# Performance work log

Hardware: AMD Instinct MI355X
Metric: run time of the kernel (lower is better)

The kernel has to match this reference:

```python
import jax, jax.numpy as jnp
import numpy as np

HIDDEN = 1024
NUM_HEADS = 16
INDEXER_HEADS = 4
D_IDX = 32
K_BASE = 512
K_MIN = 32
K_MAX = 1024
ROPE_BASE = 10000
SINK = 4


def setup_inputs() -> dict:
    key = jax.random.key(0)
    ks = jax.random.split(key, 12)
    std = 0.02
    B, T, C = 1, 2048, HIDDEN
    inp = {
        "x": jax.random.normal(ks[0], (B, T, C), jnp.float32),
        "W_Iq": jax.random.normal(ks[1], (INDEXER_HEADS * D_IDX, C), jnp.float32) * std,
        "W_Ik": jax.random.normal(ks[2], (INDEXER_HEADS * D_IDX, C), jnp.float32) * std,
        "W_Iw": jax.random.normal(ks[3], (INDEXER_HEADS, C), jnp.float32) * std,
        "gate_bias": jnp.zeros((INDEXER_HEADS,), jnp.float32),
        "head_importance_bias": jnp.zeros((NUM_HEADS,), jnp.float32),
        "W_q": jax.random.normal(ks[4], (C, C), jnp.float32) * std,
        "W_k": jax.random.normal(ks[5], (C, C), jnp.float32) * std,
        "W_v": jax.random.normal(ks[6], (C, C), jnp.float32) * std,
        "W_gv": jax.random.normal(ks[7], (C, C), jnp.float32) * std,
        "W_go": jax.random.normal(ks[8], (C, C), jnp.float32) * std,
        "W_o": jax.random.normal(ks[9], (C, C), jnp.float32) * std,
    }
    return inp


def _apply_rotary(x, cos_e, sin_e):
    # x: [B,T,H,hd]; cos_e/sin_e: [1,T,1,hd/2] (the [..., ::2] slice of cat(freqs,freqs))
    x1, x2 = x[..., ::2], x[..., 1::2]
    return jnp.concatenate((x1 * cos_e - x2 * sin_e, x1 * sin_e + x2 * cos_e), axis=-1)


def _gsa_forward(x, W_Iq, W_Ik, W_Iw, gate_bias, head_importance_bias,
                 W_q, W_k, W_v, W_gv, W_go, W_o):
    B, T, C = x.shape
    H = NUM_HEADS
    HI = INDEXER_HEADS
    hd = C // H
    hpi = H // HI

    # ----- lightning indexer -----
    q_I = (x @ W_Iq.T).reshape(B, T, HI, D_IDX)
    k_I = (x @ W_Ik.T).reshape(B, T, HI, D_IDX)
    w = jax.nn.sigmoid(x @ W_Iw.T)                       # [B,T,HI]

    match_logits = jnp.einsum('bqhd,bkhd->bhqk', q_I, k_I)  # [B,HI,T,T]
    match_logits = match_logits + gate_bias[None, :, None, None]
    match_gate = jax.nn.sigmoid(match_logits)
    w_exp = jnp.transpose(w, (0, 2, 1))[..., None]       # [B,HI,T,1]
    imp_per_indexer = w_exp * match_gate                 # [B,HI,T,T]

    importance = jnp.repeat(imp_per_indexer, hpi, axis=1)  # [B,H,T,T]
    importance = importance * jax.nn.sigmoid(head_importance_bias)[None, :, None, None]

    pos = jnp.arange(T)
    causal = pos[:, None] >= pos[None, :]                # [T,T]
    imp_masked = jnp.where(causal[None, None], importance, 0.0)

    # adaptive k_t (eval path: variance_ema == 1.0)
    var_t = jnp.var(imp_masked, axis=-1)                 # [B,H,T], biased
    k_t = jnp.clip(jnp.floor(K_BASE * var_t / 1.0), K_MIN, K_MAX).astype(jnp.int32)

    imp_sel = jnp.where(causal[None, None], importance, -jnp.inf)
    if T > SINK:
        imp_sel = imp_sel.at[..., :SINK].set(jnp.inf)    # attention sinks always selected

    # static k_limit upper bound (>= torch's dynamic min(T, max(k_t.max(), sink)));
    # entries past k_t are masked out by keep_in_topk, so result is identical
    k_limit = min(T, K_MAX)
    _, top_idx = jax.lax.top_k(imp_sel, k_limit)         # [B,H,T,k_limit]
    keep = jnp.arange(k_limit)[None, None, None, :] < k_t[..., None]

    b_ix = jnp.arange(B)[:, None, None, None]
    h_ix = jnp.arange(H)[None, :, None, None]
    q_ix = jnp.arange(T)[None, None, :, None]
    sel = jnp.zeros((B, H, T, T), bool).at[b_ix, h_ix, q_ix, top_idx].set(keep)
    sel = sel & causal[None, None]

    # ----- main attention -----
    q = (x @ W_q.T).reshape(B, T, H, hd)
    k = (x @ W_k.T).reshape(B, T, H, hd)
    v = (x @ W_v.T) * jax.nn.sigmoid(x @ W_gv.T)
    v = v.reshape(B, T, H, hd)

    inv_freq = 1.0 / (ROPE_BASE ** (jnp.arange(0, hd, 2, dtype=jnp.float32) / hd))
    freqs = jnp.outer(jnp.arange(T, dtype=jnp.float32), inv_freq)   # [T,hd/2]
    emb = jnp.concatenate((freqs, freqs), axis=-1)                  # [T,hd]
    cos_e = jnp.cos(emb)[:, ::2][None, :, None, :].astype(x.dtype)  # [1,T,1,hd/2]
    sin_e = jnp.sin(emb)[:, ::2][None, :, None, :].astype(x.dtype)
    q = _apply_rotary(q, cos_e, sin_e)
    k = _apply_rotary(k, cos_e, sin_e)

    q = jnp.transpose(q, (0, 2, 1, 3))  # [B,H,T,hd]
    k = jnp.transpose(k, (0, 2, 1, 3))
    v = jnp.transpose(v, (0, 2, 1, 3))

    min_val = jnp.finfo(q.dtype).min
    bias = jnp.where(sel, jnp.array(0.0, q.dtype), min_val)
    scores = jnp.einsum('bhqd,bhkd->bhqk', q, k) / jnp.sqrt(jnp.array(hd, q.dtype)) + bias
    attn = jax.nn.softmax(scores, axis=-1)
    o = jnp.einsum('bhqk,bhkd->bhqd', attn, v)
    o = jnp.transpose(o, (0, 2, 1, 3)).reshape(B, T, C)

    g_o = jax.nn.sigmoid(x @ W_go.T)
    return (o * g_o) @ W_o.T


def reference(x, W_Iq, W_Ik, W_Iw, gate_bias, head_importance_bias,
              W_q, W_k, W_v, W_gv, W_go, W_o):
    return _gsa_forward(x, W_Iq, W_Ik, W_Iw, gate_bias, head_importance_bias,
                        W_q, W_k, W_v, W_gv, W_go, W_o)
```

## Files before the change

kernel.cpp:

```cpp
#include <hip/hip_runtime.h>
#include <math.h>

#define T_SEQ 2048
#define C_DIM 1024
#define NH    16
#define HD    64
#define HIN   4
#define DI    32
#define SINKN 4
#define KMINV 32
#define KMAXV 1024
#define NCAT  5120
#define IMPH  2228224

typedef __bf16 bf16x8 __attribute__((ext_vector_type(8)));
typedef float  f32x4  __attribute__((ext_vector_type(4)));

__device__ __forceinline__ float sigf(float x) { return 1.f / (1.f + expf(-x)); }

__device__ __forceinline__ unsigned short f2bf(float f) {
    unsigned u = __float_as_uint(f);
    unsigned r = (u + 0x7FFFu + ((u >> 16) & 1u)) >> 16;
    return (unsigned short)r;
}

__device__ __forceinline__ float bflo(unsigned u) { return __uint_as_float(u << 16); }
__device__ __forceinline__ float bfhi(unsigned u) { return __uint_as_float(u & 0xFFFF0000u); }
__device__ __forceinline__ float bf16f(unsigned short u) { return __uint_as_float((unsigned)u << 16); }

__device__ __forceinline__ void gload16(const unsigned short* g, unsigned short* l) {
    __builtin_amdgcn_global_load_lds(
        (const __attribute__((address_space(1))) unsigned int*)(const unsigned int*)g,
        (__attribute__((address_space(3))) unsigned int*)(unsigned int*)l,
        16, 0, 0);
}

template<bool OUT_BF16>
__global__ __launch_bounds__(256) void gemm_bf16_kernel(
    const unsigned short* __restrict__ A, const unsigned short* __restrict__ B,
    void* __restrict__ Cv, int ldc)
{
    __shared__ unsigned short Asl[128 * 64];
    __shared__ unsigned short Bsl[128 * 64];
    const int K = C_DIM;
    const int tid = threadIdx.x;
    const int w = tid >> 6, lane = tid & 63;
    const int wm = w >> 1, wn = w & 1;
    const int m0 = blockIdx.y * 128, n0 = blockIdx.x * 128;

    const f32x4 z4 = {0.f, 0.f, 0.f, 0.f};
    f32x4 acc[4][4];
#pragma unroll
    for (int i = 0; i < 4; ++i)
#pragma unroll
        for (int j = 0; j < 4; ++j) acc[i][j] = z4;

    const int lrow  = w * 8 + (lane >> 3);
    const int lslot = (lane & 7) ^ (lane >> 3);
    const unsigned short* Ag = A + (size_t)(m0 + lrow) * K + lslot * 8;
    const unsigned short* Bg = B + (size_t)(n0 + lrow) * K + lslot * 8;

    const int fr = lane & 15;
    const int kg = lane >> 4;

    for (int kt = 0; kt < K; kt += 64) {
        __syncthreads();
#pragma unroll
        for (int i = 0; i < 4; ++i) {
            gload16(Ag + (size_t)(i * 32) * K + kt, &Asl[(i * 32 + w * 8) * 64]);
            gload16(Bg + (size_t)(i * 32) * K + kt, &Bsl[(i * 32 + w * 8) * 64]);
        }
        __syncthreads();
#pragma unroll
        for (int ks = 0; ks < 2; ++ks) {
            bf16x8 af[4], bfr[4];
            const int aslot = ks * 4 + kg;
#pragma unroll
            for (int f = 0; f < 4; ++f) {
                const int arow = wm * 64 + f * 16 + fr;
                af[f] = *(const bf16x8*)&Asl[arow * 64 + ((aslot ^ (arow & 7)) * 8)];
                const int brow = wn * 64 + f * 16 + fr;
                bfr[f] = *(const bf16x8*)&Bsl[brow * 64 + ((aslot ^ (brow & 7)) * 8)];
            }
#pragma unroll
            for (int mi = 0; mi < 4; ++mi)
#pragma unroll
                for (int ni = 0; ni < 4; ++ni)
                    acc[mi][ni] = __builtin_amdgcn_mfma_f32_16x16x32_bf16(
                        af[mi], bfr[ni], acc[mi][ni], 0, 0, 0);
        }
    }

#pragma unroll
    for (int mi = 0; mi < 4; ++mi) {
        const int row = m0 + wm * 64 + mi * 16 + (lane >> 4) * 4;
#pragma unroll
        for (int ni = 0; ni < 4; ++ni) {
            const int col = n0 + wn * 64 + ni * 16 + (lane & 15);
            if constexpr (OUT_BF16) {
                unsigned short* cp = (unsigned short*)Cv + (size_t)row * ldc + col;
#pragma unroll
                for (int r = 0; r < 4; ++r) cp[(size_t)r * ldc] = f2bf(acc[mi][ni][r]);
            } else {
                float* cp = (float*)Cv + (size_t)row * ldc + col;
#pragma unroll
                for (int r = 0; r < 4; ++r) cp[(size_t)r * ldc] = acc[mi][ni][r];
            }
        }
    }
}

__global__ __launch_bounds__(256) void convert_all_kernel(
    const float* __restrict__ x,
    const float* __restrict__ Wq, const float* __restrict__ Wk, const float* __restrict__ Wv,
    const float* __restrict__ Wgv, const float* __restrict__ Wgo, const float* __restrict__ Wo,
    unsigned short* __restrict__ xb, unsigned short* __restrict__ Wcatb,
    unsigned short* __restrict__ Wob)
{
    const int b = blockIdx.x;
    const float* s; unsigned short* d; size_t off;
    if (b < 2048)      { s = x;  d = xb;  off = (size_t)b * 1024; }
    else if (b < 7168) {
        const int wsel = (b - 2048) >> 10;
        switch (wsel) {
            case 0: s = Wq;  break;
            case 1: s = Wk;  break;
            case 2: s = Wv;  break;
            case 3: s = Wgv; break;
            default: s = Wgo; break;
        }
        d = Wcatb + ((size_t)wsel << 20);
        off = (size_t)((b - 2048) & 1023) * 1024;
    } else             { s = Wo; d = Wob; off = (size_t)(b - 7168) * 1024; }

    const size_t i = off + threadIdx.x * 4;
    const float4 v = *(const float4*)(s + i);
    ushort4 o;
    o.x = f2bf(v.x); o.y = f2bf(v.y); o.z = f2bf(v.z); o.w = f2bf(v.w);
    *(ushort4*)(d + i) = o;
}

__global__ void proj_w_kernel(const float* __restrict__ x, const float* __restrict__ WIw,
                              float* __restrict__ wsig)
{
    const int idx4 = blockIdx.x * 256 + threadIdx.x;
    const int part = idx4 & 3;
    const int oidx = idx4 >> 2;
    const int t = oidx >> 2, hi = oidx & 3;
    const float4* xr = (const float4*)(x + (size_t)t * C_DIM + part * 256);
    const float4* wr = (const float4*)(WIw + (size_t)hi * C_DIM + part * 256);
    float s = 0.f;
#pragma unroll
    for (int i = 0; i < 64; ++i) {
        float4 a = xr[i], b = wr[i];
        s += a.x * b.x + a.y * b.y + a.z * b.z + a.w * b.w;
    }
    s += __shfl_xor(s, 1);
    s += __shfl_xor(s, 2);
    if (part == 0) wsig[oidx] = sigf(s);
}

__global__ void rope_table_kernel(float* __restrict__ cost, float* __restrict__ sint)
{
    const int idx = blockIdx.x * 256 + threadIdx.x;
    const int t = idx >> 5, i = idx & 31;
    const int j = (2 * i) & 31;
    const float invf = powf(10000.f, -(float)j / 32.f);
    const float f = (float)t * invf;
    float sv, cv;
    sincosf(f, &sv, &cv);
    cost[idx] = cv;
    sint[idx] = sv;
}

__global__ __launch_bounds__(256) void qik_splitk_kernel(
    const float* __restrict__ x, const float* __restrict__ WIq, const float* __restrict__ WIk,
    float* __restrict__ part)
{
    const int which = blockIdx.x;
    const int s = blockIdx.y;
    const int mt = blockIdx.z;
    const float* B = which ? WIk : WIq;
    const int m0 = mt * 128;
    const int kb = s * 128;

    __shared__ float As[16][132];
    __shared__ float Bs[16][132];
    const int tid = threadIdx.x;
    const int tx = tid & 15, ty = tid >> 4;

    float acc[8][8];
#pragma unroll
    for (int i = 0; i < 8; ++i)
#pragma unroll
        for (int j = 0; j < 8; ++j) acc[i][j] = 0.f;

    const int sr = tid >> 1;
    const int sk = (tid & 1) * 8;
    const float* Ap = x + (size_t)(m0 + sr) * C_DIM + kb + sk;
    const float* Bp = B + (size_t)sr * C_DIM + kb + sk;

    for (int k0 = 0; k0 < 128; k0 += 16) {
        float4 a0 = *(const float4*)(Ap + k0);
        float4 a1 = *(const float4*)(Ap + k0 + 4);
        float4 b0 = *(const float4*)(Bp + k0);
        float4 b1 = *(const float4*)(Bp + k0 + 4);
        __syncthreads();
        As[sk + 0][sr] = a0.x; As[sk + 1][sr] = a0.y; As[sk + 2][sr] = a0.z; As[sk + 3][sr] = a0.w;
        As[sk + 4][sr] = a1.x; As[sk + 5][sr] = a1.y; As[sk + 6][sr] = a1.z; As[sk + 7][sr] = a1.w;
        Bs[sk + 0][sr] = b0.x; Bs[sk + 1][sr] = b0.y; Bs[sk + 2][sr] = b0.z; Bs[sk + 3][sr] = b0.w;
        Bs[sk + 4][sr] = b1.x; Bs[sk + 5][sr] = b1.y; Bs[sk + 6][sr] = b1.z; Bs[sk + 7][sr] = b1.w;
        __syncthreads();
#pragma unroll
        for (int kk = 0; kk < 16; ++kk) {
            float4 aA = *(const float4*)&As[kk][ty * 4];
            float4 aB = *(const float4*)&As[kk][64 + ty * 4];
            float4 bA = *(const float4*)&Bs[kk][tx * 4];
            float4 bB = *(const float4*)&Bs[kk][64 + tx * 4];
            float am[8] = {aA.x, aA.y, aA.z, aA.w, aB.x, aB.y, aB.z, aB.w};
            float bn[8] = {bA.x, bA.y, bA.z, bA.w, bB.x, bB.y, bB.z, bB.w};
#pragma unroll
            for (int i = 0; i < 8; ++i)
#pragma unroll
                for (int j = 0; j < 8; ++j) acc[i][j] = fmaf(am[i], bn[j], acc[i][j]);
        }
    }

    float* cp0 = part + (size_t)(which * 8 + s) * T_SEQ * 128;
#pragma unroll
    for (int ih = 0; ih < 2; ++ih)
#pragma unroll
        for (int i = 0; i < 4; ++i) {
            const int row = m0 + ih * 64 + ty * 4 + i;
            float* cp = cp0 + (size_t)row * 128;
            float4 v0 = make_float4(acc[ih*4+i][0], acc[ih*4+i][1], acc[ih*4+i][2], acc[ih*4+i][3]);
            float4 v1 = make_float4(acc[ih*4+i][4], acc[ih*4+i][5], acc[ih*4+i][6], acc[ih*4+i][7]);
            *(float4*)(cp + tx * 4) = v0;
            *(float4*)(cp + 64 + tx * 4) = v1;
        }
}

__global__ void qik_reduce_kernel(const float* __restrict__ part,
                                  float* __restrict__ qI, float* __restrict__ kI)
{
    const int idx = blockIdx.x * 256 + threadIdx.x;
    const int which = idx >> 18;
    const int e = idx & 262143;
    const float* p = part + (size_t)which * 8 * T_SEQ * 128 + e;
    float s = 0.f;
#pragma unroll
    for (int j = 0; j < 8; ++j) s += p[(size_t)j * T_SEQ * 128];
    (which ? kI : qI)[e] = s;
}

__global__ void rope_v_kernel(
    const unsigned short* __restrict__ lincatb,
    const float* __restrict__ cost, const float* __restrict__ sint,
    float* __restrict__ Q, unsigned short* __restrict__ Kb, unsigned short* __restrict__ Vb)
{
    const int idx = blockIdx.x * 256 + threadIdx.x;
    const int i = idx & 31;
    const int h = (idx >> 5) & 15;
    const int t = idx >> 9;
    const float cv = cost[t * 32 + i], sv = sint[t * 32 + i];
    const size_t src = (size_t)t * NCAT + h * HD + 2 * i;
    const ushort2 q2 = *(const ushort2*)(lincatb + src);
    const ushort2 k2 = *(const ushort2*)(lincatb + src + 1024);
    const ushort2 v2 = *(const ushort2*)(lincatb + src + 2048);
    const ushort2 g2 = *(const ushort2*)(lincatb + src + 3072);
    const float qx = bf16f(q2.x), qy = bf16f(q2.y);
    const float kx = bf16f(k2.x), ky = bf16f(k2.y);
    const float vx = bf16f(v2.x), vy = bf16f(v2.y);
    const float gx = bf16f(g2.x), gy = bf16f(g2.y);
    const size_t dst = ((size_t)h * T_SEQ + t) * HD;
    Q[dst + i]      = qx * cv - qy * sv;
    Q[dst + 32 + i] = qx * sv + qy * cv;
    Kb[dst + i]      = f2bf(kx * cv - ky * sv);
    Kb[dst + 32 + i] = f2bf(kx * sv + ky * cv);
    ushort2 vo;
    vo.x = f2bf(vx * sigf(gx));
    vo.y = f2bf(vy * sigf(gy));
    *(ushort2*)(Vb + dst + 2 * i) = vo;
}

__global__ __launch_bounds__(256) void impA_kernel(
    const float* __restrict__ qI, const float* __restrict__ kI,
    const float* __restrict__ wsig, const float* __restrict__ gate_bias,
    float* __restrict__ imp)
{
    const int t = blockIdx.x;
    const int hi = blockIdx.y;
    int qi = (int)((sqrtf(8.f * (float)t + 1.f) - 1.f) * 0.5f);
    if ((qi + 1) * (qi + 2) / 2 <= t) qi++;
    if (qi * (qi + 1) / 2 > t) qi--;
    const int ki = t - qi * (qi + 1) / 2;
    const int m0 = qi * 128;

    __shared__ float As[32][132];
    __shared__ float Bs[32][132];
    const int tid = threadIdx.x;
    const int tx = tid & 15, ty = tid >> 4;

    {
        const int sr = tid >> 1;
        const int sk = (tid & 1) * 16;
        const float4* Ap = (const float4*)(qI + (size_t)(m0 + sr) * 128 + hi * 32 + sk);
        const float4* Bp = (const float4*)(kI + (size_t)(ki * 128 + sr) * 128 + hi * 32 + sk);
#pragma unroll
        for (int j4 = 0; j4 < 4; ++j4) {
            float4 a = Ap[j4], b = Bp[j4];
            As[sk + j4*4 + 0][sr] = a.x; As[sk + j4*4 + 1][sr] = a.y;
            As[sk + j4*4 + 2][sr] = a.z; As[sk + j4*4 + 3][sr] = a.w;
            Bs[sk + j4*4 + 0][sr] = b.x; Bs[sk + j4*4 + 1][sr] = b.y;
            Bs[sk + j4*4 + 2][sr] = b.z; Bs[sk + j4*4 + 3][sr] = b.w;
        }
    }
    __syncthreads();

    float acc[8][8];
#pragma unroll
    for (int i = 0; i < 8; ++i)
#pragma unroll
        for (int j = 0; j < 8; ++j) acc[i][j] = 0.f;

#pragma unroll
    for (int kk = 0; kk < 32; ++kk) {
        float4 aA = *(const float4*)&As[kk][ty * 4];
        float4 aB = *(const float4*)&As[kk][64 + ty * 4];
        float4 bA = *(const float4*)&Bs[kk][tx * 4];
        float4 bB = *(const float4*)&Bs[kk][64 + tx * 4];
        float am[8] = {aA.x, aA.y, aA.z, aA.w, aB.x, aB.y, aB.z, aB.w};
        float bn[8] = {bA.x, bA.y, bA.z, bA.w, bB.x, bB.y, bB.z, bB.w};
#pragma unroll
        for (int i = 0; i < 8; ++i)
#pragma unroll
            for (int j = 0; j < 8; ++j) acc[i][j] = fmaf(am[i], bn[j], acc[i][j]);
    }

    const float gb = gate_bias[hi];
    const size_t rw = (size_t)(qi + 1) * 128;
    float* impb = imp + (size_t)hi * IMPH + (size_t)16384 * (qi * (qi + 1) / 2) + ki * 128;
#pragma unroll
    for (int ih = 0; ih < 2; ++ih)
#pragma unroll
        for (int i = 0; i < 4; ++i) {
            const int rr = ih * 64 + ty * 4 + i;
            const float wr = wsig[(m0 + rr) * 4 + hi];
            float* cp = impb + (size_t)rr * rw;
            float4 v0, v1;
            v0.x = wr * sigf(acc[ih*4+i][0] + gb);
            v0.y = wr * sigf(acc[ih*4+i][1] + gb);
            v0.z = wr * sigf(acc[ih*4+i][2] + gb);
            v0.w = wr * sigf(acc[ih*4+i][3] + gb);
            v1.x = wr * sigf(acc[ih*4+i][4] + gb);
            v1.y = wr * sigf(acc[ih*4+i][5] + gb);
            v1.z = wr * sigf(acc[ih*4+i][6] + gb);
            v1.w = wr * sigf(acc[ih*4+i][7] + gb);
            *(float4*)(cp + tx * 4) = v0;
            *(float4*)(cp + 64 + tx * 4) = v1;
        }
}

template<int NC>
__device__ __forceinline__ void impB_body(
    const float* __restrict__ imp, const float* __restrict__ head_bias,
    unsigned short* __restrict__ sidxg, unsigned* __restrict__ cnts,
    int q, int hi, int lane)
{
    const int qc = q >> 6;
    const unsigned long long lmask_lt = (lane == 0) ? 0ull : ((~0ull) >> (64 - lane));

    const int qi = q >> 7;
    const size_t rw = (size_t)(qi + 1) * 128;
    const float* row = imp + (size_t)hi * IMPH +
                       (size_t)16384 * (qi * (qi + 1) / 2) + (size_t)(q - qi * 128) * rw;

    unsigned ordv[NC];
    double dsum = 0.0, dsq = 0.0;
#pragma unroll
    for (int i = 0; i < NC; ++i) {
        const int k = i * 64 + lane;
        unsigned vb = 0u;
        if (i <= qc) {
            const float v = row[k];
            const bool causal = (k <= q);
            const float vm = causal ? v : 0.f;
            dsum += (double)vm;
            dsq  += (double)vm * (double)vm;
            vb = causal ? __float_as_uint(v) : 0u;
        }
        if (i == 0 && lane < SINKN) vb = 0x7F800000u;
        ordv[i] = vb;
    }

#pragma unroll
    for (int off = 1; off < 64; off <<= 1) {
        dsum += __shfl_xor(dsum, off);
        dsq  += __shfl_xor(dsq, off);
    }

    int kts[4];
#pragma unroll
    for (int j = 0; j < 4; ++j) {
        const float sh = sigf(head_bias[hi * 4 + j]);
        const double mean = dsum / (double)T_SEQ;
        double var = dsq / (double)T_SEQ - mean * mean;
        if (var < 0.0) var = 0.0;
        const double vh = var * (double)sh * (double)sh;
        int kt = (int)floor(512.0 * vh);
        kt = kt < KMINV ? KMINV : (kt > KMAXV ? KMAXV : kt);
        kts[j] = kt;
    }

    unsigned vs[4]; int tt[4];
#pragma unroll
    for (int j = 0; j < 4; ++j) {
        bool dup = false;
#pragma unroll
        for (int p = 0; p < 4; ++p) {
            if (p < j && !dup && kts[p] == kts[j]) { vs[j] = vs[p]; tt[j] = tt[p]; dup = true; }
        }
        if (!dup) {
            const int kt = kts[j];
            unsigned X = 0;
#pragma unroll 1
            for (int b = 30; b >= 0; --b) {
                const unsigned Xt = X | (1u << b);
                int c = 0;
#pragma unroll
                for (int i = 0; i < NC; ++i)
                    c += (int)__popcll(__ballot(ordv[i] >= Xt));
                if (c >= kt) X = Xt;
            }
            int cg = 0;
#pragma unroll
            for (int i = 0; i < NC; ++i)
                cg += (int)__popcll(__ballot(ordv[i] > X));
            vs[j] = X; tt[j] = kt - cg;
        }
    }

    unsigned cnt = 0;
    unsigned short* sp = sidxg + ((size_t)hi * T_SEQ + q) * KMAXV;
    const bool uni = (kts[0] == kts[1]) && (kts[1] == kts[2]) && (kts[2] == kts[3]);

    if (uni) {
        int eqr = 0;
        const unsigned v0 = vs[0]; const int t0 = tt[0];
#pragma unroll
        for (int i = 0; i < NC; ++i) {
            const int k = i * 64 + lane;
            const unsigned x = ordv[i];
            const bool eq = (x == v0);
            const unsigned long long beq = __ballot(eq);
            const bool sel = (x > v0) || (eq && (eqr + (int)__popcll(beq & lmask_lt) < t0));
            eqr += (int)__popcll(beq);
            const bool valid = (k <= q) && sel;
            const unsigned long long bv = __ballot(valid);
            if (valid) {
                const unsigned pos = cnt + (unsigned)__popcll(bv & lmask_lt);
                if (pos < KMAXV) sp[pos] = (unsigned short)((unsigned)k | (0xFu << 11));
            }
            cnt += (unsigned)__popcll(bv);
        }
    } else {
        int eqr0 = 0, eqr1 = 0, eqr2 = 0, eqr3 = 0;
#pragma unroll
        for (int i = 0; i < NC; ++i) {
            const int k = i * 64 + lane;
            const unsigned x = ordv[i];
            unsigned mask = 0;
            {
                const bool eq = (x == vs[0]);
                const unsigned long long beq = __ballot(eq);
                const bool sel = (x > vs[0]) || (eq && (eqr0 + (int)__popcll(beq & lmask_lt) < tt[0]));
                eqr0 += (int)__popcll(beq);
                if (sel) mask |= 1u;
            }
            {
                const bool eq = (x == vs[1]);
                const unsigned long long beq = __ballot(eq);
                const bool sel = (x > vs[1]) || (eq && (eqr1 + (int)__popcll(beq & lmask_lt) < tt[1]));
                eqr1 += (int)__popcll(beq);
                if (sel) mask |= 2u;
            }
            {
                const bool eq = (x == vs[2]);
                const unsigned long long beq = __ballot(eq);
                const bool sel = (x > vs[2]) || (eq && (eqr2 + (int)__popcll(beq & lmask_lt) < tt[2]));
                eqr2 += (int)__popcll(beq);
                if (sel) mask |= 4u;
            }
            {
                const bool eq = (x == vs[3]);
                const unsigned long long beq = __ballot(eq);
                const bool sel = (x > vs[3]) || (eq && (eqr3 + (int)__popcll(beq & lmask_lt) < tt[3]));
                eqr3 += (int)__popcll(beq);
                if (sel) mask |= 8u;
            }
            const bool valid = (k <= q) && (mask != 0u);
            const unsigned long long bv = __ballot(valid);
            if (valid) {
                const unsigned pos = cnt + (unsigned)__popcll(bv & lmask_lt);
                if (pos < KMAXV) sp[pos] = (unsigned short)((unsigned)k | (mask << 11));
            }
            cnt += (unsigned)__popcll(bv);
        }
    }
    if (lane == 0) cnts[(size_t)hi * T_SEQ + q] = cnt < KMAXV ? cnt : KMAXV;
}

__global__ __launch_bounds__(256) void impB_kernel(
    const float* __restrict__ imp, const float* __restrict__ head_bias,
    unsigned short* __restrict__ sidxg, unsigned* __restrict__ cnts)
{
    const int wv = threadIdx.x >> 6;
    const int lane = threadIdx.x & 63;
    const int hi = blockIdx.y;
    const int band = 7 - (blockIdx.x >> 6);
    const int bx = blockIdx.x & 63;
    const int q = band * 256 + bx * 4 + wv;
    switch (band) {
        case 0:  impB_body< 4>(imp, head_bias, sidxg, cnts, q, hi, lane); break;
        case 1:  impB_body< 8>(imp, head_bias, sidxg, cnts, q, hi, lane); break;
        case 2:  impB_body<12>(imp, head_bias, sidxg, cnts, q, hi, lane); break;
        case 3:  impB_body<16>(imp, head_bias, sidxg, cnts, q, hi, lane); break;
        case 4:  impB_body<20>(imp, head_bias, sidxg, cnts, q, hi, lane); break;
        case 5:  impB_body<24>(imp, head_bias, sidxg, cnts, q, hi, lane); break;
        case 6:  impB_body<28>(imp, head_bias, sidxg, cnts, q, hi, lane); break;
        default: impB_body<32>(imp, head_bias, sidxg, cnts, q, hi, lane); break;
    }
}

__global__ __launch_bounds__(256) void attn_sparse_kernel(
    const float* __restrict__ Q, const unsigned short* __restrict__ Kb,
    const unsigned short* __restrict__ Vb,
    const unsigned short* __restrict__ sidx, const unsigned* __restrict__ cnts,
    const unsigned short* __restrict__ lincatb, unsigned short* __restrict__ ogb)
{
    const int orig = blockIdx.x + (blockIdx.y << 8);
    const int c = ((orig & 7) << 9) | (orig >> 3);
    const int h = c >> 8;
    const int qt = c & 255;
    const int hi = h >> 2, hj = h & 3;
    const int wv = threadIdx.x >> 6;
    const int lane = threadIdx.x & 63;
    const int qh = lane >> 5;
    const int l32 = lane & 31;
    const int kk = l32 >> 2;
    const int dg = lane & 3;
    const int q = qt * 8 + wv * 2 + qh;

    const size_t hq = (size_t)hi * T_SEQ + q;
    const int nv = (int)cnts[hq];
    const int nvm = max(nv, __shfl_xor(nv, 32));
    const unsigned short* sp = sidx + hq * KMAXV;
    const unsigned short* Kh = Kb + (size_t)h * T_SEQ * HD + dg * 16;
    const unsigned short* Vh = Vb + (size_t)h * T_SEQ * HD + dg * 16;

    float4 qg[4];
    {
        const float4* qp = (const float4*)(Q + ((size_t)h * T_SEQ + q) * HD + dg * 16);
        qg[0] = qp[0]; qg[1] = qp[1]; qg[2] = qp[2]; qg[3] = qp[3];
    }

    float acc[16];
#pragma unroll
    for (int i = 0; i < 16; ++i) acc[i] = 0.f;
    float l = 0.f;

    if (nvm <= 32) {
        const ushort4 e4 = *(const ushort4*)(sp + kk * 4);
        const unsigned ev[4] = {e4.x, e4.y, e4.z, e4.w};

        float s[4]; int idxs[4];
#pragma unroll
        for (int sub = 0; sub < 4; ++sub) {
            const int kpos = kk * 4 + sub;
            const unsigned e = ev[sub];
            const bool ok = (kpos < nv) && ((e >> (11 + hj)) & 1u);
            const int iv = ok ? (int)(e & 0x7FFu) : 0;
            idxs[sub] = iv;
            const uint4* kr = (const uint4*)(Kh + (size_t)iv * HD);
// ... 107 lines not shown
            }
        }
    }

#pragma unroll
    for (int i = 0; i < 16; ++i) {
        acc[i] += __shfl_xor(acc[i], 4);
        acc[i] += __shfl_xor(acc[i], 8);
        acc[i] += __shfl_xor(acc[i], 16);
    }
    const float invl = 1.f / l;
    float oval0 = acc[0], oval1 = acc[1];
#pragma unroll
    for (int i = 1; i < 8; ++i)
        if (kk == i) { oval0 = acc[2 * i]; oval1 = acc[2 * i + 1]; }
    const int d0 = dg * 16 + kk * 2;
    const ushort2 g2 = *(const ushort2*)(lincatb + (size_t)q * NCAT + 4096 + h * HD + d0);
    ushort2 o2;
    o2.x = f2bf(oval0 * invl * sigf(bf16f(g2.x)));
    o2.y = f2bf(oval1 * invl * sigf(bf16f(g2.y)));
    *(ushort2*)(ogb + (size_t)q * C_DIM + h * HD + d0) = o2;
}

extern "C" void kernel_launch(void* const* d_in, const int* in_sizes, int n_in,
                              void* d_out, int out_size, void* d_ws, size_t ws_size,
                              hipStream_t stream)
{
    const float* x   = (const float*)d_in[0];
    const float* WIq = (const float*)d_in[1];
    const float* WIk = (const float*)d_in[2];
    const float* WIw = (const float*)d_in[3];
    const float* gb  = (const float*)d_in[4];
    const float* hib = (const float*)d_in[5];
    const float* Wq  = (const float*)d_in[6];
    const float* Wk  = (const float*)d_in[7];
    const float* Wv  = (const float*)d_in[8];
    const float* Wgv = (const float*)d_in[9];
    const float* Wgo = (const float*)d_in[10];
    const float* Wo  = (const float*)d_in[11];
    float* out = (float*)d_out;

    char* ws = (char*)d_ws;
    const size_t MB = 1024 * 1024;
    float*    qI     = (float*)(ws + 0 * MB);
    float*    kI     = (float*)(ws + 1 * MB);
    float*    wsig   = (float*)(ws + 2 * MB);
    unsigned* cnts   = (unsigned*)(ws + 2 * MB + 64 * 1024);
    float*    cost   = (float*)(ws + 2 * MB + 512 * 1024);
    float*    sint   = (float*)(ws + 2 * MB + 768 * 1024);
    float*    Q      = (float*)(ws + 3 * MB);
    unsigned short* Kb = (unsigned short*)(ws + 11 * MB);
    unsigned short* Vb = (unsigned short*)(ws + 15 * MB);
    unsigned short* sidx = (unsigned short*)(ws + 19 * MB);
    float*    part    = (float*)(ws + 35 * MB);
    float*    imp     = (float*)(ws + 35 * MB);
    unsigned short* lincatb = (unsigned short*)(ws + 35 * MB);
    unsigned short* ogb   = (unsigned short*)(ws + 75 * MB);
    unsigned short* xb    = (unsigned short*)(ws + 79 * MB);
    unsigned short* Wcatb = (unsigned short*)(ws + 83 * MB);
    unsigned short* Wob   = (unsigned short*)(ws + 93 * MB);

    rope_table_kernel<<<dim3(256), 256, 0, stream>>>(cost, sint);
    qik_splitk_kernel<<<dim3(2, 8, 16), 256, 0, stream>>>(x, WIq, WIk, part);
    qik_reduce_kernel<<<dim3(2048), 256, 0, stream>>>(part, qI, kI);
    proj_w_kernel<<<dim3(128), 256, 0, stream>>>(x, WIw, wsig);
    impA_kernel<<<dim3(136, 4), 256, 0, stream>>>(qI, kI, wsig, gb, imp);
    impB_kernel<<<dim3(512, 4), 256, 0, stream>>>(imp, hib, sidx, cnts);
    convert_all_kernel<<<dim3(8192), 256, 0, stream>>>(
        x, Wq, Wk, Wv, Wgv, Wgo, Wo, xb, Wcatb, Wob);
    gemm_bf16_kernel<true><<<dim3(40, 16), 256, 0, stream>>>(xb, Wcatb, lincatb, NCAT);
    rope_v_kernel<<<dim3(4096), 256, 0, stream>>>(lincatb, cost, sint, Q, Kb, Vb);
    attn_sparse_kernel<<<dim3(256, 16), 256, 0, stream>>>(Q, Kb, Vb, sidx, cnts, lincatb, ogb);
    gemm_bf16_kernel<false><<<dim3(8, 16), 256, 0, stream>>>(ogb, Wob, out, C_DIM);
}
```

Before: 194.9 us.

## Merge independent stage kernels into heterogeneous block-dispatch launches

Independent kernels are combined into three launches that dispatch on block index: rope table, indexer split-K, the w projection and bf16 conversion go into pre_kernel; the QKV GEMM and indexer importance GEMM go into mid_kernel; top-k selection and rope/V packing go into sel_kernel. Workspace buffers are moved so that concurrently running stages no longer alias each other. The aim is to cut launch gaps and let small stages fill idle CUs alongside bigger ones. In exchange, each merged kernel uses the union of the stages' shared memory and register needs, which can lower occupancy.

```diff
diff --git a/kernel.cpp b/kernel.cpp
--- a/kernel.cpp
+++ b/kernel.cpp
@@ -36,17 +36,18 @@
 }
 
 template<bool OUT_BF16>
-__global__ __launch_bounds__(256) void gemm_bf16_kernel(
+__device__ __forceinline__ void gemm_body(
+    char* smemc,
     const unsigned short* __restrict__ A, const unsigned short* __restrict__ B,
-    void* __restrict__ Cv, int ldc)
-{
-    __shared__ unsigned short Asl[128 * 64];
-    __shared__ unsigned short Bsl[128 * 64];
+    void* __restrict__ Cv, int ldc, int bx, int by)
+{
+    unsigned short* Asl = (unsigned short*)smemc;
+    unsigned short* Bsl = (unsigned short*)(smemc + 16384);
     const int K = C_DIM;
     const int tid = threadIdx.x;
     const int w = tid >> 6, lane = tid & 63;
     const int wm = w >> 1, wn = w & 1;
-    const int m0 = blockIdx.y * 128, n0 = blockIdx.x * 128;
+    const int m0 = by * 128, n0 = bx * 128;
 
     const f32x4 z4 = {0.f, 0.f, 0.f, 0.f};
     f32x4 acc[4][4];
@@ -110,14 +111,21 @@
     }
 }
 
-__global__ __launch_bounds__(256) void convert_all_kernel(
-    const float* __restrict__ x,
+__global__ __launch_bounds__(256) void gemm_out_kernel(
+    const unsigned short* __restrict__ A, const unsigned short* __restrict__ B,
+    float* __restrict__ C, int ldc)
+{
+    __shared__ __align__(16) char smem[32768];
+    gemm_body<false>(smem, A, B, C, ldc, blockIdx.x, blockIdx.y);
+}
+
+__device__ __forceinline__ void convert_body(
+    int b, const float* __restrict__ x,
     const float* __restrict__ Wq, const float* __restrict__ Wk, const float* __restrict__ Wv,
     const float* __restrict__ Wgv, const float* __restrict__ Wgo, const float* __restrict__ Wo,
     unsigned short* __restrict__ xb, unsigned short* __restrict__ Wcatb,
     unsigned short* __restrict__ Wob)
 {
-    const int b = blockIdx.x;
     const float* s; unsigned short* d; size_t off;
     if (b < 2048)      { s = x;  d = xb;  off = (size_t)b * 1024; }
     else if (b < 7168) {
@@ -140,10 +148,11 @@
     *(ushort4*)(d + i) = o;
 }
 
-__global__ void proj_w_kernel(const float* __restrict__ x, const float* __restrict__ WIw,
-                              float* __restrict__ wsig)
-{
-    const int idx4 = blockIdx.x * 256 + threadIdx.x;
+__device__ __forceinline__ void proj_w_body(
+    int b, const float* __restrict__ x, const float* __restrict__ WIw,
+    float* __restrict__ wsig)
+{
+    const int idx4 = b * 256 + threadIdx.x;
     const int part = idx4 & 3;
     const int oidx = idx4 >> 2;
     const int t = oidx >> 2, hi = oidx & 3;
@@ -152,17 +161,18 @@
     float s = 0.f;
 #pragma unroll
     for (int i = 0; i < 64; ++i) {
-        float4 a = xr[i], b = wr[i];
-        s += a.x * b.x + a.y * b.y + a.z * b.z + a.w * b.w;
+        float4 a = xr[i], w4 = wr[i];
+        s += a.x * w4.x + a.y * w4.y + a.z * w4.z + a.w * w4.w;
     }
     s += __shfl_xor(s, 1);
     s += __shfl_xor(s, 2);
     if (part == 0) wsig[oidx] = sigf(s);
 }
 
-__global__ void rope_table_kernel(float* __restrict__ cost, float* __restrict__ sint)
-{
-    const int idx = blockIdx.x * 256 + threadIdx.x;
+__device__ __forceinline__ void rope_table_body(
+    int b, float* __restrict__ cost, float* __restrict__ sint)
+{
+    const int idx = b * 256 + threadIdx.x;
     const int t = idx >> 5, i = idx & 31;
     const int j = (2 * i) & 31;
     const float invf = powf(10000.f, -(float)j / 32.f);
@@ -173,19 +183,16 @@
     sint[idx] = sv;
 }
 
-__global__ __launch_bounds__(256) void qik_splitk_kernel(
+__device__ __forceinline__ void qik_body(
+    char* smemc, int which, int s, int mt,
     const float* __restrict__ x, const float* __restrict__ WIq, const float* __restrict__ WIk,
     float* __restrict__ part)
 {
-    const int which = blockIdx.x;
-    const int s = blockIdx.y;
-    const int mt = blockIdx.z;
+    float (*As)[132] = (float(*)[132])smemc;
+    float (*Bs)[132] = (float(*)[132])(smemc + 8448);
     const float* B = which ? WIk : WIq;
     const int m0 = mt * 128;
     const int kb = s * 128;
-
-    __shared__ float As[16][132];
-    __shared__ float Bs[16][132];
     const int tid = threadIdx.x;
     const int tx = tid & 15, ty = tid >> 4;
 
@@ -240,6 +247,29 @@
         }
 }
 
+__global__ __launch_bounds__(256) void pre_kernel(
+    const float* __restrict__ x,
+    const float* __restrict__ WIq, const float* __restrict__ WIk, const float* __restrict__ WIw,
+    const float* __restrict__ Wq, const float* __restrict__ Wk, const float* __restrict__ Wv,
+    const float* __restrict__ Wgv, const float* __restrict__ Wgo, const float* __restrict__ Wo,
+    unsigned short* __restrict__ xb, unsigned short* __restrict__ Wcatb,
+    unsigned short* __restrict__ Wob,
+    float* __restrict__ part, float* __restrict__ wsig,
+    float* __restrict__ cost, float* __restrict__ sint)
+{
+    __shared__ __align__(16) char smem[16896];
+    const int b = blockIdx.x;
+    if (b < 256) {
+        qik_body(smem, b & 1, (b >> 1) & 7, b >> 4, x, WIq, WIk, part);
+    } else if (b < 512) {
+        rope_table_body(b - 256, cost, sint);
+    } else if (b < 640) {
+        proj_w_body(b - 512, x, WIw, wsig);
+    } else {
+        convert_body(b - 640, x, Wq, Wk, Wv, Wgv, Wgo, Wo, xb, Wcatb, Wob);
+    }
+}
+
 __global__ void qik_reduce_kernel(const float* __restrict__ part,
                                   float* __restrict__ qI, float* __restrict__ kI)
 {
@@ -253,12 +283,255 @@
     (which ? kI : qI)[e] = s;
 }
 
-__global__ void rope_v_kernel(
-    const unsigned short* __restrict__ lincatb,
+__device__ __forceinline__ void impA_body(
+    char* smemc,
+    const float* __restrict__ qI, const float* __restrict__ kI,
+    const float* __restrict__ wsig, const float* __restrict__ gate_bias,
+    float* __restrict__ imp, int t, int hi)
+{
+    float (*As)[132] = (float(*)[132])smemc;
+    float (*Bs)[132] = (float(*)[132])(smemc + 16896);
+    int qi = (int)((sqrtf(8.f * (float)t + 1.f) - 1.f) * 0.5f);
+    if ((qi + 1) * (qi + 2) / 2 <= t) qi++;
+    if (qi * (qi + 1) / 2 > t) qi--;
+    const int ki = t - qi * (qi + 1) / 2;
+    const int m0 = qi * 128;
+
+    const int tid = threadIdx.x;
+    const int tx = tid & 15, ty = tid >> 4;
+
+    {
+        const int sr = tid >> 1;
+        const int sk = (tid & 1) * 16;
+        const float4* Ap = (const float4*)(qI + (size_t)(m0 + sr) * 128 + hi * 32 + sk);
+        const float4* Bp = (const float4*)(kI + (size_t)(ki * 128 + sr) * 128 + hi * 32 + sk);
+#pragma unroll
+        for (int j4 = 0; j4 < 4; ++j4) {
+            float4 a = Ap[j4], b = Bp[j4];
+            As[sk + j4*4 + 0][sr] = a.x; As[sk + j4*4 + 1][sr] = a.y;
+            As[sk + j4*4 + 2][sr] = a.z; As[sk + j4*4 + 3][sr] = a.w;
+            Bs[sk + j4*4 + 0][sr] = b.x; Bs[sk + j4*4 + 1][sr] = b.y;
+            Bs[sk + j4*4 + 2][sr] = b.z; Bs[sk + j4*4 + 3][sr] = b.w;
+        }
+    }
+    __syncthreads();
+
+    float acc[8][8];
+#pragma unroll
+    for (int i = 0; i < 8; ++i)
+#pragma unroll
+        for (int j = 0; j < 8; ++j) acc[i][j] = 0.f;
+
+#pragma unroll
+    for (int kk = 0; kk < 32; ++kk) {
+        float4 aA = *(const float4*)&As[kk][ty * 4];
+        float4 aB = *(const float4*)&As[kk][64 + ty * 4];
+        float4 bA = *(const float4*)&Bs[kk][tx * 4];
+        float4 bB = *(const float4*)&Bs[kk][64 + tx * 4];
+        float am[8] = {aA.x, aA.y, aA.z, aA.w, aB.x, aB.y, aB.z, aB.w};
+        float bn[8] = {bA.x, bA.y, bA.z, bA.w, bB.x, bB.y, bB.z, bB.w};
+#pragma unroll
+        for (int i = 0; i < 8; ++i)
+#pragma unroll
+            for (int j = 0; j < 8; ++j) acc[i][j] = fmaf(am[i], bn[j], acc[i][j]);
+    }
+
+    const float gb = gate_bias[hi];
+    const size_t rw = (size_t)(qi + 1) * 128;
+    float* impb = imp + (size_t)hi * IMPH + (size_t)16384 * (qi * (qi + 1) / 2) + ki * 128;
+#pragma unroll
+    for (int ih = 0; ih < 2; ++ih)
+#pragma unroll
+        for (int i = 0; i < 4; ++i) {
+            const int rr = ih * 64 + ty * 4 + i;
+            const float wr = wsig[(m0 + rr) * 4 + hi];
+            float* cp = impb + (size_t)rr * rw;
+            float4 v0, v1;
+            v0.x = wr * sigf(acc[ih*4+i][0] + gb);
+            v0.y = wr * sigf(acc[ih*4+i][1] + gb);
+            v0.z = wr * sigf(acc[ih*4+i][2] + gb);
+            v0.w = wr * sigf(acc[ih*4+i][3] + gb);
+            v1.x = wr * sigf(acc[ih*4+i][4] + gb);
+            v1.y = wr * sigf(acc[ih*4+i][5] + gb);
+            v1.z = wr * sigf(acc[ih*4+i][6] + gb);
+            v1.w = wr * sigf(acc[ih*4+i][7] + gb);
+            *(float4*)(cp + tx * 4) = v0;
+            *(float4*)(cp + 64 + tx * 4) = v1;
+        }
+}
+
+__global__ __launch_bounds__(256) void mid_kernel(
+    const unsigned short* __restrict__ xb, const unsigned short* __restrict__ Wcatb,
+    unsigned short* __restrict__ lincatb,
+    const float* __restrict__ qI, const float* __restrict__ kI,
+    const float* __restrict__ wsig, const float* __restrict__ gate_bias,
+    float* __restrict__ imp)
+{
+    __shared__ __align__(16) char smem[33792];
+    const int b = blockIdx.x;
+    if (b < 640) {
+        gemm_body<true>(smem, xb, Wcatb, lincatb, NCAT, b % 40, b / 40);
+    } else {
+        const int bb = b - 640;
+        impA_body(smem, qI, kI, wsig, gate_bias, imp, bb % 136, bb / 136);
+    }
+}
+
+template<int NC>
+__device__ __forceinline__ void impB_body(
+    const float* __restrict__ imp, const float* __restrict__ head_bias,
+    unsigned short* __restrict__ sidxg, unsigned* __restrict__ cnts,
+    int q, int hi, int lane)
+{
+    const int qc = q >> 6;
+    const unsigned long long lmask_lt = (lane == 0) ? 0ull : ((~0ull) >> (64 - lane));
+
+    const int qi = q >> 7;
+    const size_t rw = (size_t)(qi + 1) * 128;
+    const float* row = imp + (size_t)hi * IMPH +
+                       (size_t)16384 * (qi * (qi + 1) / 2) + (size_t)(q - qi * 128) * rw;
+
+    unsigned ordv[NC];
+    double dsum = 0.0, dsq = 0.0;
+#pragma unroll
+    for (int i = 0; i < NC; ++i) {
+        const int k = i * 64 + lane;
+        unsigned vb = 0u;
+        if (i <= qc) {
+            const float v = row[k];
+            const bool causal = (k <= q);
+            const float vm = causal ? v : 0.f;
+            dsum += (double)vm;
+            dsq  += (double)vm * (double)vm;
+            vb = causal ? __float_as_uint(v) : 0u;
+        }
+        if (i == 0 && lane < SINKN) vb = 0x7F800000u;
+        ordv[i] = vb;
+    }
+
+#pragma unroll
+    for (int off = 1; off < 64; off <<= 1) {
+        dsum += __shfl_xor(dsum, off);
+        dsq  += __shfl_xor(dsq, off);
+    }
+
+    int kts[4];
+#pragma unroll
+    for (int j = 0; j < 4; ++j) {
+        const float sh = sigf(head_bias[hi * 4 + j]);
+        const double mean = dsum / (double)T_SEQ;
+        double var = dsq / (double)T_SEQ - mean * mean;
+        if (var < 0.0) var = 0.0;
+        const double vh = var * (double)sh * (double)sh;
+        int kt = (int)floor(512.0 * vh);
+        kt = kt < KMINV ? KMINV : (kt > KMAXV ? KMAXV : kt);
+        kts[j] = kt;
+    }
+
+    unsigned vs[4]; int tt[4];
+#pragma unroll
+    for (int j = 0; j < 4; ++j) {
+        bool dup = false;
+#pragma unroll
+        for (int p = 0; p < 4; ++p) {
+            if (p < j && !dup && kts[p] == kts[j]) { vs[j] = vs[p]; tt[j] = tt[p]; dup = true; }
+        }
+        if (!dup) {
+            const int kt = kts[j];
+            unsigned X = 0;
+#pragma unroll 1
+            for (int b = 30; b >= 0; --b) {
+                const unsigned Xt = X | (1u << b);
+                int c = 0;
+#pragma unroll
+                for (int i = 0; i < NC; ++i)
+                    c += (int)__popcll(__ballot(ordv[i] >= Xt));
+                if (c >= kt) X = Xt;
+            }
+            int cg = 0;
+#pragma unroll
+            for (int i = 0; i < NC; ++i)
+                cg += (int)__popcll(__ballot(ordv[i] > X));
+            vs[j] = X; tt[j] = kt - cg;
+        }
+    }
+
+    unsigned cnt = 0;
+    unsigned short* sp = sidxg + ((size_t)hi * T_SEQ + q) * KMAXV;
+    const bool uni = (kts[0] == kts[1]) && (kts[1] == kts[2]) && (kts[2] == kts[3]);
+
+    if (uni) {
+        int eqr = 0;
+        const unsigned v0 = vs[0]; const int t0 = tt[0];
+#pragma unroll
+        for (int i = 0; i < NC; ++i) {
+            const int k = i * 64 + lane;
+            const unsigned x = ordv[i];
+            const bool eq = (x == v0);
+            const unsigned long long beq = __ballot(eq);
+            const bool sel = (x > v0) || (eq && (eqr + (int)__popcll(beq & lmask_lt) < t0));
+            eqr += (int)__popcll(beq);
+            const bool valid = (k <= q) && sel;
+            const unsigned long long bv = __ballot(valid);
+            if (valid) {
+                const unsigned pos = cnt + (unsigned)__popcll(bv & lmask_lt);
+                if (pos < KMAXV) sp[pos] = (unsigned short)((unsigned)k | (0xFu << 11));
+            }
+            cnt += (unsigned)__popcll(bv);
+        }
+    } else {
+        int eqr0 = 0, eqr1 = 0, eqr2 = 0, eqr3 = 0;
+#pragma unroll
+        for (int i = 0; i < NC; ++i) {
+            const int k = i * 64 + lane;
+            const unsigned x = ordv[i];
+            unsigned mask = 0;
+            {
+                const bool eq = (x == vs[0]);
+                const unsigned long long beq = __ballot(eq);
+                const bool sel = (x > vs[0]) || (eq && (eqr0 + (int)__popcll(beq & lmask_lt) < tt[0]));
+                eqr0 += (int)__popcll(beq);
+                if (sel) mask |= 1u;
+            }
+            {
+                const bool eq = (x == vs[1]);
+                const unsigned long long beq = __ballot(eq);
+                const bool sel = (x > vs[1]) || (eq && (eqr1 + (int)__popcll(beq & lmask_lt) < tt[1]));
+                eqr1 += (int)__popcll(beq);
+                if (sel) mask |= 2u;
+            }
+            {
+                const bool eq = (x == vs[2]);
+                const unsigned long long beq = __ballot(eq);
+                const bool sel = (x > vs[2]) || (eq && (eqr2 + (int)__popcll(beq & lmask_lt) < tt[2]));
+                eqr2 += (int)__popcll(beq);
+                if (sel) mask |= 4u;
+            }
+            {
+                const bool eq = (x == vs[3]);
+                const unsigned long long beq = __ballot(eq);
+                const bool sel = (x > vs[3]) || (eq && (eqr3 + (int)__popcll(beq & lmask_lt) < tt[3]));
+                eqr3 += (int)__popcll(beq);
+                if (sel) mask |= 8u;
+            }
+            const bool valid = (k <= q) && (mask != 0u);
+            const unsigned long long bv = __ballot(valid);
+            if (valid) {
+                const unsigned pos = cnt + (unsigned)__popcll(bv & lmask_lt);
+                if (pos < KMAXV) sp[pos] = (unsigned short)((unsigned)k | (mask << 11));
+            }
+            cnt += (unsigned)__popcll(bv);
+        }
+    }
+    if (lane == 0) cnts[(size_t)hi * T_SEQ + q] = cnt < KMAXV ? cnt : KMAXV;
+}
+
+__device__ __forceinline__ void rope_v_body(
+    int b, const unsigned short* __restrict__ lincatb,
     const float* __restrict__ cost, const float* __restrict__ sint,
     float* __restrict__ Q, unsigned short* __restrict__ Kb, unsigned short* __restrict__ Vb)
 {
-    const int idx = blockIdx.x * 256 + threadIdx.x;
+    const int idx = b * 256 + threadIdx.x;
     const int i = idx & 31;
     const int h = (idx >> 5) & 15;
     const int t = idx >> 9;
@@ -283,252 +556,34 @@
     *(ushort2*)(Vb + dst + 2 * i) = vo;
 }
 
-__global__ __launch_bounds__(256) void impA_kernel(
-    const float* __restrict__ qI, const float* __restrict__ kI,
-    const float* __restrict__ wsig, const float* __restrict__ gate_bias,
-    float* __restrict__ imp)
-{
-    const int t = blockIdx.x;
-    const int hi = blockIdx.y;
-    int qi = (int)((sqrtf(8.f * (float)t + 1.f) - 1.f) * 0.5f);
-    if ((qi + 1) * (qi + 2) / 2 <= t) qi++;
-    if (qi * (qi + 1) / 2 > t) qi--;
-    const int ki = t - qi * (qi + 1) / 2;
-    const int m0 = qi * 128;
-
-    __shared__ float As[32][132];
-    __shared__ float Bs[32][132];
-    const int tid = threadIdx.x;
-    const int tx = tid & 15, ty = tid >> 4;
-
-    {
-        const int sr = tid >> 1;
-        const int sk = (tid & 1) * 16;
-        const float4* Ap = (const float4*)(qI + (size_t)(m0 + sr) * 128 + hi * 32 + sk);
-        const float4* Bp = (const float4*)(kI + (size_t)(ki * 128 + sr) * 128 + hi * 32 + sk);
-#pragma unroll
-        for (int j4 = 0; j4 < 4; ++j4) {
-            float4 a = Ap[j4], b = Bp[j4];
-            As[sk + j4*4 + 0][sr] = a.x; As[sk + j4*4 + 1][sr] = a.y;
-            As[sk + j4*4 + 2][sr] = a.z; As[sk + j4*4 + 3][sr] = a.w;
-            Bs[sk + j4*4 + 0][sr] = b.x; Bs[sk + j4*4 + 1][sr] = b.y;
-            Bs[sk + j4*4 + 2][sr] = b.z; Bs[sk + j4*4 + 3][sr] = b.w;
-        }
-    }
-    __syncthreads();
-
-    float acc[8][8];
-#pragma unroll
-    for (int i = 0; i < 8; ++i)
-#pragma unroll
-        for (int j = 0; j < 8; ++j) acc[i][j] = 0.f;
-
-#pragma unroll
-    for (int kk = 0; kk < 32; ++kk) {
-        float4 aA = *(const float4*)&As[kk][ty * 4];
-        float4 aB = *(const float4*)&As[kk][64 + ty * 4];
-        float4 bA = *(const float4*)&Bs[kk][tx * 4];
-        float4 bB = *(const float4*)&Bs[kk][64 + tx * 4];
-        float am[8] = {aA.x, aA.y, aA.z, aA.w, aB.x, aB.y, aB.z, aB.w};
-        float bn[8] = {bA.x, bA.y, bA.z, bA.w, bB.x, bB.y, bB.z, bB.w};
-#pragma unroll
-        for (int i = 0; i < 8; ++i)
-#pragma unroll
-            for (int j = 0; j < 8; ++j) acc[i][j] = fmaf(am[i], bn[j], acc[i][j]);
-    }
-
-    const float gb = gate_bias[hi];
-    const size_t rw = (size_t)(qi + 1) * 128;
-    float* impb = imp + (size_t)hi * IMPH + (size_t)16384 * (qi * (qi + 1) / 2) + ki * 128;
-#pragma unroll
-    for (int ih = 0; ih < 2; ++ih)
-#pragma unroll
-        for (int i = 0; i < 4; ++i) {
-            const int rr = ih * 64 + ty * 4 + i;
-            const float wr = wsig[(m0 + rr) * 4 + hi];
-            float* cp = impb + (size_t)rr * rw;
-            float4 v0, v1;
-            v0.x = wr * sigf(acc[ih*4+i][0] + gb);
-            v0.y = wr * sigf(acc[ih*4+i][1] + gb);
-            v0.z = wr * sigf(acc[ih*4+i][2] + gb);
-            v0.w = wr * sigf(acc[ih*4+i][3] + gb);
-            v1.x = wr * sigf(acc[ih*4+i][4] + gb);
-            v1.y = wr * sigf(acc[ih*4+i][5] + gb);
-            v1.z = wr * sigf(acc[ih*4+i][6] + gb);
-            v1.w = wr * sigf(acc[ih*4+i][7] + gb);
-            *(float4*)(cp + tx * 4) = v0;
-            *(float4*)(cp + 64 + tx * 4) = v1;
-        }
-}
-
-template<int NC>
-__device__ __forceinline__ void impB_body(
+__global__ __launch_bounds__(256) void sel_kernel(
     const float* __restrict__ imp, const float* __restrict__ head_bias,
     unsigned short* __restrict__ sidxg, unsigned* __restrict__ cnts,
-    int q, int hi, int lane)
-{
-    const int qc = q >> 6;
-    const unsigned long long lmask_lt = (lane == 0) ? 0ull : ((~0ull) >> (64 - lane));
-
-    const int qi = q >> 7;
-    const size_t rw = (size_t)(qi + 1) * 128;
-    const float* row = imp + (size_t)hi * IMPH +
-                       (size_t)16384 * (qi * (qi + 1) / 2) + (size_t)(q - qi * 128) * rw;
-
-    unsigned ordv[NC];
-    double dsum = 0.0, dsq = 0.0;
-#pragma unroll
-    for (int i = 0; i < NC; ++i) {
-        const int k = i * 64 + lane;
-        unsigned vb = 0u;
-        if (i <= qc) {
-            const float v = row[k];
-            const bool causal = (k <= q);
-            const float vm = causal ? v : 0.f;
-            dsum += (double)vm;
-            dsq  += (double)vm * (double)vm;
-            vb = causal ? __float_as_uint(v) : 0u;
-        }
-        if (i == 0 && lane < SINKN) vb = 0x7F800000u;
-        ordv[i] = vb;
-    }
-
-#pragma unroll
-    for (int off = 1; off < 64; off <<= 1) {
-        dsum += __shfl_xor(dsum, off);
-        dsq  += __shfl_xor(dsq, off);
-    }
-
-    int kts[4];
-#pragma unroll
-    for (int j = 0; j < 4; ++j) {
-        const float sh = sigf(head_bias[hi * 4 + j]);
-        const double mean = dsum / (double)T_SEQ;
-        double var = dsq / (double)T_SEQ - mean * mean;
-        if (var < 0.0) var = 0.0;
-        const double vh = var * (double)sh * (double)sh;
-        int kt = (int)floor(512.0 * vh);
-        kt = kt < KMINV ? KMINV : (kt > KMAXV ? KMAXV : kt);
-        kts[j] = kt;
-    }
-
-    unsigned vs[4]; int tt[4];
-#pragma unroll
-    for (int j = 0; j < 4; ++j) {
-        bool dup = false;
-#pragma unroll
-        for (int p = 0; p < 4; ++p) {
-            if (p < j && !dup && kts[p] == kts[j]) { vs[j] = vs[p]; tt[j] = tt[p]; dup = true; }
-        }
-        if (!dup) {
-            const int kt = kts[j];
-            unsigned X = 0;
-#pragma unroll 1
-            for (int b = 30; b >= 0; --b) {
-                const unsigned Xt = X | (1u << b);
-                int c = 0;
-#pragma unroll
-                for (int i = 0; i < NC; ++i)
-                    c += (int)__popcll(__ballot(ordv[i] >= Xt));
-                if (c >= kt) X = Xt;
-            }
-            int cg = 0;
-#pragma unroll
-            for (int i = 0; i < NC; ++i)
-                cg += (int)__popcll(__ballot(ordv[i] > X));
-            vs[j] = X; tt[j] = kt - cg;
-        }
-    }
-
-    unsigned cnt = 0;
-    unsigned short* sp = sidxg + ((size_t)hi * T_SEQ + q) * KMAXV;
-    const bool uni = (kts[0] == kts[1]) && (kts[1] == kts[2]) && (kts[2] == kts[3]);
-
-    if (uni) {
-        int eqr = 0;
-        const unsigned v0 = vs[0]; const int t0 = tt[0];
-#pragma unroll
-        for (int i = 0; i < NC; ++i) {
-            const int k = i * 64 + lane;
-            const unsigned x = ordv[i];
-            const bool eq = (x == v0);
-            const unsigned long long beq = __ballot(eq);
-            const bool sel = (x > v0) || (eq && (eqr + (int)__popcll(beq & lmask_lt) < t0));
-            eqr += (int)__popcll(beq);
-            const bool valid = (k <= q) && sel;
-            const unsigned long long bv = __ballot(valid);
-            if (valid) {
-                const unsigned pos = cnt + (unsigned)__popcll(bv & lmask_lt);
-                if (pos < KMAXV) sp[pos] = (unsigned short)((unsigned)k | (0xFu << 11));
-            }
-            cnt += (unsigned)__popcll(bv);
+    const unsigned short* __restrict__ lincatb,
+    const float* __restrict__ cost, const float* __restrict__ sint,
+    float* __restrict__ Q, unsigned short* __restrict__ Kb, unsigned short* __restrict__ Vb)
+{
+    const int b = blockIdx.x;
+    if (b < 2048) {
+        const int bx = b & 511;
+        const int hi = b >> 9;
+        const int wv = threadIdx.x >> 6;
+        const int lane = threadIdx.x & 63;
+        const int band = 7 - (bx >> 6);
+        const int bxx = bx & 63;
+        const int q = band * 256 + bxx * 4 + wv;
+        switch (band) {
+            case 0:  impB_body< 4>(imp, head_bias, sidxg, cnts, q, hi, lane); break;
+            case 1:  impB_body< 8>(imp, head_bias, sidxg, cnts, q, hi, lane); break;
+            case 2:  impB_body<12>(imp, head_bias, sidxg, cnts, q, hi, lane); break;
+            case 3:  impB_body<16>(imp, head_bias, sidxg, cnts, q, hi, lane); break;
+            case 4:  impB_body<20>(imp, head_bias, sidxg, cnts, q, hi, lane); break;
+            case 5:  impB_body<24>(imp, head_bias, sidxg, cnts, q, hi, lane); break;
+            case 6:  impB_body<28>(imp, head_bias, sidxg, cnts, q, hi, lane); break;
+            default: impB_body<32>(imp, head_bias, sidxg, cnts, q, hi, lane); break;
         }
     } else {
-        int eqr0 = 0, eqr1 = 0, eqr2 = 0, eqr3 = 0;
-#pragma unroll
-        for (int i = 0; i < NC; ++i) {
-            const int k = i * 64 + lane;
-            const unsigned x = ordv[i];
-            unsigned mask = 0;
-            {
-                const bool eq = (x == vs[0]);
-                const unsigned long long beq = __ballot(eq);
-                const bool sel = (x > vs[0]) || (eq && (eqr0 + (int)__popcll(beq & lmask_lt) < tt[0]));
-                eqr0 += (int)__popcll(beq);
-                if (sel) mask |= 1u;
-            }
-            {
-                const bool eq = (x == vs[1]);
-                const unsigned long long beq = __ballot(eq);
-                const bool sel = (x > vs[1]) || (eq && (eqr1 + (int)__popcll(beq & lmask_lt) < tt[1]));
-                eqr1 += (int)__popcll(beq);
-                if (sel) mask |= 2u;
-            }
-            {
-                const bool eq = (x == vs[2]);
-                const unsigned long long beq = __ballot(eq);
-                const bool sel = (x > vs[2]) || (eq && (eqr2 + (int)__popcll(beq & lmask_lt) < tt[2]));
-                eqr2 += (int)__popcll(beq);
-                if (sel) mask |= 4u;
-            }
-            {
-                const bool eq = (x == vs[3]);
-                const unsigned long long beq = __ballot(eq);
-                const bool sel = (x > vs[3]) || (eq && (eqr3 + (int)__popcll(beq & lmask_lt) < tt[3]));
-                eqr3 += (int)__popcll(beq);
-                if (sel) mask |= 8u;
-            }
-            const bool valid = (k <= q) && (mask != 0u);
-            const unsigned long long bv = __ballot(valid);
-            if (valid) {
-                const unsigned pos = cnt + (unsigned)__popcll(bv & lmask_lt);
-                if (pos < KMAXV) sp[pos] = (unsigned short)((unsigned)k | (mask << 11));
-            }
-            cnt += (unsigned)__popcll(bv);
-        }
-    }
-    if (lane == 0) cnts[(size_t)hi * T_SEQ + q] = cnt < KMAXV ? cnt : KMAXV;
-}
-
-__global__ __launch_bounds__(256) void impB_kernel(
-    const float* __restrict__ imp, const float* __restrict__ head_bias,
-    unsigned short* __restrict__ sidxg, unsigned* __restrict__ cnts)
-{
-    const int wv = threadIdx.x >> 6;
-    const int lane = threadIdx.x & 63;
-    const int hi = blockIdx.y;
-    const int band = 7 - (blockIdx.x >> 6);
-    const int bx = blockIdx.x & 63;
-    const int q = band * 256 + bx * 4 + wv;
-    switch (band) {
-        case 0:  impB_body< 4>(imp, head_bias, sidxg, cnts, q, hi, lane); break;
-        case 1:  impB_body< 8>(imp, head_bias, sidxg, cnts, q, hi, lane); break;
-        case 2:  impB_body<12>(imp, head_bias, sidxg, cnts, q, hi, lane); break;
-        case 3:  impB_body<16>(imp, head_bias, sidxg, cnts, q, hi, lane); break;
-        case 4:  impB_body<20>(imp, head_bias, sidxg, cnts, q, hi, lane); break;
-        case 5:  impB_body<24>(imp, head_bias, sidxg, cnts, q, hi, lane); break;
-        case 6:  impB_body<28>(imp, head_bias, sidxg, cnts, q, hi, lane); break;
-        default: impB_body<32>(imp, head_bias, sidxg, cnts, q, hi, lane); break;
+        rope_v_body(b - 2048, lincatb, cost, sint, Q, Kb, Vb);
     }
 }
 
@@ -742,24 +797,22 @@
     unsigned short* Kb = (unsigned short*)(ws + 11 * MB);
     unsigned short* Vb = (unsigned short*)(ws + 15 * MB);
     unsigned short* sidx = (unsigned short*)(ws + 19 * MB);
-    float*    part    = (float*)(ws + 35 * MB);
     float*    imp     = (float*)(ws + 35 * MB);
-    unsigned short* lincatb = (unsigned short*)(ws + 35 * MB);
-    unsigned short* ogb   = (unsigned short*)(ws + 75 * MB);
-    unsigned short* xb    = (unsigned short*)(ws + 79 * MB);
-    unsigned short* Wcatb = (unsigned short*)(ws + 83 * MB);
-    unsigned short* Wob   = (unsigned short*)(ws + 93 * MB);
-
-    rope_table_kernel<<<dim3(256), 256, 0, stream>>>(cost, sint);
-    qik_splitk_kernel<<<dim3(2, 8, 16), 256, 0, stream>>>(x, WIq, WIk, part);
+    float*    part    = (float*)(ws + 71 * MB);
+    unsigned short* lincatb = (unsigned short*)(ws + 71 * MB);
+    unsigned short* ogb   = (unsigned short*)(ws + 91 * MB);
+    unsigned short* xb    = (unsigned short*)(ws + 95 * MB);
+    unsigned short* Wcatb = (unsigned short*)(ws + 99 * MB);
+    unsigned short* Wob   = (unsigned short*)(ws + 109 * MB);
+
+    pre_kernel<<<dim3(8832), 256, 0, stream>>>(
+        x, WIq, WIk, WIw, Wq, Wk, Wv, Wgv, Wgo, Wo,
+        xb, Wcatb, Wob, part, wsig, cost, sint);
     qik_reduce_kernel<<<dim3(2048), 256, 0, stream>>>(part, qI, kI);
-    proj_w_kernel<<<dim3(128), 256, 0, stream>>>(x, WIw, wsig);
-    impA_kernel<<<dim3(136, 4), 256, 0, stream>>>(qI, kI, wsig, gb, imp);
-    impB_kernel<<<dim3(512, 4), 256, 0, stream>>>(imp, hib, sidx, cnts);
-    convert_all_kernel<<<dim3(8192), 256, 0, stream>>>(
-        x, Wq, Wk, Wv, Wgv, Wgo, Wo, xb, Wcatb, Wob);
-    gemm_bf16_kernel<true><<<dim3(40, 16), 256, 0, stream>>>(xb, Wcatb, lincatb, NCAT);
-    rope_v_kernel<<<dim3(4096), 256, 0, stream>>>(lincatb, cost, sint, Q, Kb, Vb);
+    mid_kernel<<<dim3(1184), 256, 0, stream>>>(
+        xb, Wcatb, lincatb, qI, kI, wsig, gb, imp);
+    sel_kernel<<<dim3(6144), 256, 0, stream>>>(
+        imp, hib, sidx, cnts, lincatb, cost, sint, Q, Kb, Vb);
     attn_sparse_kernel<<<dim3(256, 16), 256, 0, stream>>>(Q, Kb, Vb, sidx, cnts, lincatb, ogb);
-    gemm_bf16_kernel<false><<<dim3(8, 16), 256, 0, stream>>>(ogb, Wob, out, C_DIM);
-}
+    gemm_out_kernel<<<dim3(8, 16), 256, 0, stream>>>(ogb, Wob, out, C_DIM);
+}
```

Measured after the change: 163.9 us. 15.9% less time.
